# Performance work log

Measured on AMD Instinct MI355X. Metric: run time of the kernel, lower is better.

The kernel has to match this reference:

```python
import jax, jax.numpy as jnp
import numpy as np
import math

D_KEY = 64
SCALE = math.sqrt(D_KEY)
INF = 1e10  # finite stand-in for the original INF constant
CAUSAL = True
DIAG = False


def setup_inputs() -> dict:
    key = jax.random.key(0)
    kq, kk, kv = jax.random.split(key, 3)
    B, L, D = 16, 2048, D_KEY
    return {
        "query": jax.random.normal(kq, (B, L, D), dtype=jnp.float32),
        "key": jax.random.normal(kk, (B, L, D), dtype=jnp.float32),
        "value": jax.random.normal(kv, (B, L, D), dtype=jnp.float32),
    }


def reference(query, key, value):
    # scores: [B, Lq, Lk]
    scores = jnp.einsum("bqd,bkd->bqk", query, key)
    L = key.shape[1]
    if CAUSAL:
        # subtract INF above the diagonal (strict upper triangle), as in torch triu(1)
        tri = jnp.triu(jnp.full((L, L), INF, dtype=scores.dtype), k=1)
        scores = scores - tri[None, :, :]
    if DIAG:
        # original scatters -INF onto the diagonal along dim 1
        diag_mask = jnp.eye(L, dtype=bool)
        scores = jnp.where(diag_mask[None, :, :], -INF, scores)
    # softmax over keys after scaling; dropout with p=0.0 is identity
    attn = jax.nn.softmax(scores / SCALE, axis=-1)
    return jnp.einsum("bqk,bkd->bqd", attn, value)
```

## Files before the change

kernel.cpp:

```cpp
#include <hip/hip_runtime.h>

typedef __bf16 bf16_t;
typedef __bf16 bf16x4 __attribute__((ext_vector_type(4)));
typedef __bf16 bf16x8 __attribute__((ext_vector_type(8)));
typedef float  f32x4  __attribute__((ext_vector_type(4)));

#define B_SZ  16
#define L_SEQ 2048
#define D_H   64
#define QB    64
#define KB    128

#define QSCALE 0.18033688011112043f

__global__ __launch_bounds__(256, 2)
void attn_fwd_kernel(const float* __restrict__ Qg, const float* __restrict__ Kg,
                     const float* __restrict__ Vg, float* __restrict__ Og)
{
    const int lin  = blockIdx.x;
    const int xcd  = lin & 7;
    const int slot = lin >> 3;
    const int half = slot >> 5;
    const int qi   = slot & 31;
    const int b    = xcd * 2 + half;
    const int qt   = half ? qi : (31 - qi);

    const int tid  = threadIdx.x;
    const int lane = tid & 63;
    const int lg   = lane >> 4;
    const int lc   = lane & 15;
    const int lc7  = lc & 7;

    __shared__ __align__(16) bf16_t K_lds[2][KB * D_H];
    __shared__ __align__(16) bf16_t Vt_lds[2][D_H * KB];

    const size_t bbase = (size_t)b * L_SEQ * D_H;

    const int qrow = qt * QB + (tid >> 6) * 16 + lc;
    bf16x8 qa[2];
#pragma unroll
    for (int h = 0; h < 2; ++h) {
        const float* qp = Qg + bbase + (size_t)qrow * D_H + h * 32 + lg * 8;
        const f32x4 f0 = *reinterpret_cast<const f32x4*>(qp);
        const f32x4 f1 = *reinterpret_cast<const f32x4*>(qp + 4);
        bf16x8 a;
#pragma unroll
        for (int j = 0; j < 4; ++j) { a[j] = (bf16_t)(f0[j] * QSCALE); a[4 + j] = (bf16_t)(f1[j] * QSCALE); }
        qa[h] = a;
    }

    f32x4 o[4];
#pragma unroll
    for (int dt = 0; dt < 4; ++dt) o[dt] = (f32x4){0.f, 0.f, 0.f, 0.f};
    float m = -1e30f, l = 0.f;

    const int nkt = (qt + 2) >> 1;

    const int vkb  = tid & 31;
    const int vdg  = tid >> 5;
    const int vpos = ((vkb >> 3) << 5) + ((vkb & 3) << 3) + (((vkb >> 2) & 1) << 2);

    f32x4 kreg[8], vreg[8];

    auto issueK = [&](int kt) {
        const int kbase = kt * KB;
#pragma unroll
        for (int i = 0; i < 4; ++i) {
            const int u = i * 256 + tid;
            const int r = u >> 3, ch = u & 7;
            const float* p = Kg + bbase + (size_t)(kbase + r) * D_H + ch * 8;
            kreg[2 * i]     = *reinterpret_cast<const f32x4*>(p);
            kreg[2 * i + 1] = *reinterpret_cast<const f32x4*>(p + 4);
        }
    };
    auto issueV = [&](int kt) {
        const int kbase = kt * KB;
#pragma unroll
        for (int d2 = 0; d2 < 2; ++d2)
#pragma unroll
            for (int i = 0; i < 4; ++i)
                vreg[d2 * 4 + i] = *reinterpret_cast<const f32x4*>(
                    Vg + bbase + (size_t)(kbase + vkb * 4 + i) * D_H + (vdg + d2 * 8) * 4);
    };
    auto writeK = [&](int buf) {
#pragma unroll
        for (int i = 0; i < 4; ++i) {
            const int u = i * 256 + tid;
            const int r = u >> 3, ch = u & 7;
            bf16x8 kk;
#pragma unroll
            for (int j = 0; j < 4; ++j) { kk[j] = (bf16_t)kreg[2 * i][j]; kk[4 + j] = (bf16_t)kreg[2 * i + 1][j]; }
            *reinterpret_cast<bf16x8*>(&K_lds[buf][r * 64 + ((ch ^ (r & 7)) << 3)]) = kk;
        }
    };
    auto writeV = [&](int buf) {
#pragma unroll
        for (int d2 = 0; d2 < 2; ++d2) {
            const int db = vdg + d2 * 8;
#pragma unroll
            for (int j = 0; j < 4; ++j) {
                const int d = db * 4 + j;
                bf16x4 cj = { (bf16_t)vreg[d2 * 4 + 0][j], (bf16_t)vreg[d2 * 4 + 1][j],
                              (bf16_t)vreg[d2 * 4 + 2][j], (bf16_t)vreg[d2 * 4 + 3][j] };
                const int hw = d * 128 + (((vpos >> 3) ^ (d & 7)) << 3) + (vpos & 7);
                *reinterpret_cast<bf16x4*>(&Vt_lds[buf][hw]) = cj;
            }
        }
    };

    issueK(0); issueV(0); writeK(0); writeV(0);
    __syncthreads();
    int cur = 0;
    for (int kt = 0; kt < nkt; ++kt) {
        const bool last = (kt == nkt - 1);
        const int kbase = kt * KB;
        if (!last) issueK(kt + 1);

        f32x4 sc[8];
        __builtin_amdgcn_s_setprio(1);
#pragma unroll
        for (int n = 0; n < 8; ++n) {
            f32x4 acc = (f32x4){0.f, 0.f, 0.f, 0.f};
#pragma unroll
            for (int h = 0; h < 2; ++h) {
                const int hw = (n * 16 + lc) * 64 + ((((h << 2) | lg) ^ lc7) << 3);
                const bf16x8 kb = *reinterpret_cast<const bf16x8*>(&K_lds[cur][hw]);
                acc = __builtin_amdgcn_mfma_f32_16x16x32_bf16(kb, qa[h], acc, 0, 0, 0);
            }
            sc[n] = acc;
        }
        __builtin_amdgcn_s_setprio(0);
        if (!last) issueV(kt + 1);
        if (last) {
#pragma unroll
            for (int n = 0; n < 8; ++n)
#pragma unroll
                for (int r = 0; r < 4; ++r)
                    if (kbase + n * 16 + lg * 4 + r > qrow) sc[n][r] = -1e30f;
        }

        float mxp = fmaxf(fmaxf(sc[0][0], sc[0][1]), fmaxf(sc[0][2], sc[0][3]));
#pragma unroll
        for (int n = 1; n < 8; ++n)
            mxp = fmaxf(mxp, fmaxf(fmaxf(sc[n][0], sc[n][1]), fmaxf(sc[n][2], sc[n][3])));
        if (!__all(mxp <= m + 8.0f)) {
            float mx = mxp;
            mx = fmaxf(mx, __shfl_xor(mx, 16));
            mx = fmaxf(mx, __shfl_xor(mx, 32));
            const float mn = fmaxf(m, mx);
            const float alpha = exp2f(m - mn);
            m = mn;
            l *= alpha;
#pragma unroll
            for (int dt = 0; dt < 4; ++dt)
#pragma unroll
                for (int r = 0; r < 4; ++r) o[dt][r] *= alpha;
        }
        bf16x8 w[4];
        float rs = 0.f;
#pragma unroll
        for (int n = 0; n < 8; ++n) {
            const float p0 = exp2f(sc[n][0] - m), p1 = exp2f(sc[n][1] - m);
            const float p2 = exp2f(sc[n][2] - m), p3 = exp2f(sc[n][3] - m);
            rs += (p0 + p1) + (p2 + p3);
            const int wi = n >> 1, off = (n & 1) * 4;
            w[wi][off + 0] = (bf16_t)p0; w[wi][off + 1] = (bf16_t)p1;
            w[wi][off + 2] = (bf16_t)p2; w[wi][off + 3] = (bf16_t)p3;
        }
        l += rs;

        if (!last) writeK(cur ^ 1);

        __builtin_amdgcn_s_setprio(1);
#pragma unroll
        for (int ks = 0; ks < 4; ++ks) {
#pragma unroll
            for (int dt = 0; dt < 4; ++dt) {
                const int hw = (dt * 16 + lc) * 128 + ((((ks << 2) | lg) ^ lc7) << 3);
                const bf16x8 vb = *reinterpret_cast<const bf16x8*>(&Vt_lds[cur][hw]);
                o[dt] = __builtin_amdgcn_mfma_f32_16x16x32_bf16(vb, w[ks], o[dt], 0, 0, 0);
            }
        }
        __builtin_amdgcn_s_setprio(0);

        if (!last) writeV(cur ^ 1);
        __syncthreads();
        cur ^= 1;
    }

    float lr = l;
    lr += __shfl_xor(lr, 16);
    lr += __shfl_xor(lr, 32);
    const float inv = 1.0f / lr;
#pragma unroll
    for (int dt = 0; dt < 4; ++dt) {
        f32x4 val = { o[dt][0] * inv, o[dt][1] * inv, o[dt][2] * inv, o[dt][3] * inv };
        *reinterpret_cast<f32x4*>(Og + bbase + (size_t)qrow * D_H + dt * 16 + lg * 4) = val;
    }
}

extern "C" void kernel_launch(void* const* d_in, const int* in_sizes, int n_in,
                              void* d_out, int out_size, void* d_ws, size_t ws_size,
                              hipStream_t stream)
{
    const float* Q = (const float*)d_in[0];
    const float* K = (const float*)d_in[1];
    const float* V = (const float*)d_in[2];
    float* O = (float*)d_out;
    attn_fwd_kernel<<<dim3(512), dim3(256), 0, stream>>>(Q, K, V, O);
}
```

Measured before the change: 40.14 us.

## Pre-convert K/V to swizzled bf16 images and stream them via global_load_lds

Adds a preprocessing kernel that converts K and V to bf16 once per call. It writes them into workspace already in the swizzled LDS tile layout, with V transposed. The attention kernel then copies each tile straight from global memory to LDS with global_load_lds, dropping the register staging and per-tile conversion that were repeated by every Q block. This costs an extra kernel launch and a workspace round trip, and the V transpose in the preprocess uses strided scalar reads. A fallback path keeps the original kernel for when the workspace is too small.

Result: slower. 43.28 us (+7.8%).

```diff
diff --git a/kernel.cpp b/kernel.cpp
--- a/kernel.cpp
+++ b/kernel.cpp
@@ -10,12 +10,56 @@
 #define D_H   64
 #define QB    64
 #define KB    128
+#define NTILE 16
+#define TILE_HW (KB * D_H)
 
 #define QSCALE 0.18033688011112043f
 
+#define GLD_LDS16(g, l) __builtin_amdgcn_global_load_lds(                       \
+    (const __attribute__((address_space(1))) void*)(g),                         \
+    (__attribute__((address_space(3))) void*)(l), 16, 0, 0)
+
+__global__ __launch_bounds__(256)
+void preproc_kernel(const float* __restrict__ Kg, const float* __restrict__ Vg,
+                    bf16_t* __restrict__ Kimg, bf16_t* __restrict__ Vimg)
+{
+    const int kt = blockIdx.x, b = blockIdx.y;
+    const int t  = threadIdx.x;
+    const size_t src = (size_t)b * L_SEQ * D_H + (size_t)kt * KB * D_H;
+    bf16_t* ko = Kimg + (size_t)(b * NTILE + kt) * TILE_HW;
+    bf16_t* vo = Vimg + (size_t)(b * NTILE + kt) * TILE_HW;
+
+#pragma unroll
+    for (int i = 0; i < 4; ++i) {
+        const int u = i * 256 + t, r = u >> 3, ch = u & 7;
+        const float* p = Kg + src + r * 64 + ch * 8;
+        const f32x4 a = *reinterpret_cast<const f32x4*>(p);
+        const f32x4 c = *reinterpret_cast<const f32x4*>(p + 4);
+        bf16x8 kk;
+#pragma unroll
+        for (int j = 0; j < 4; ++j) { kk[j] = (bf16_t)a[j]; kk[4 + j] = (bf16_t)c[j]; }
+        *reinterpret_cast<bf16x8*>(&ko[r * 64 + ((ch ^ (r & 7)) << 3)]) = kk;
+    }
+
+    const int d = t & 63, pcg = t >> 6;
+#pragma unroll
+    for (int i = 0; i < 4; ++i) {
+        const int pc = pcg * 4 + i;
+        bf16x8 vv;
+#pragma unroll
+        for (int pw = 0; pw < 8; ++pw) {
+            const int pos = pc * 8 + pw;
+            const int vkb = ((pos >> 3) & 3) | (((pos >> 2) & 1) << 2) | (((pos >> 5) & 3) << 3);
+            const int k   = (vkb << 2) | (pos & 3);
+            vv[pw] = (bf16_t)Vg[src + (size_t)k * 64 + d];
+        }
+        *reinterpret_cast<bf16x8*>(&vo[d * 128 + ((pc ^ (d & 7)) << 3)]) = vv;
+    }
+}
+
 __global__ __launch_bounds__(256, 2)
-void attn_fwd_kernel(const float* __restrict__ Qg, const float* __restrict__ Kg,
-                     const float* __restrict__ Vg, float* __restrict__ Og)
+void attn_fwd_kernel(const float* __restrict__ Qg, float* __restrict__ Og,
+                     const bf16_t* __restrict__ Kimg, const bf16_t* __restrict__ Vimg)
 {
     const int lin  = blockIdx.x;
     const int xcd  = lin & 7;
@@ -26,17 +70,20 @@
     const int qt   = half ? qi : (31 - qi);
 
     const int tid  = threadIdx.x;
+    const int wave = tid >> 6;
     const int lane = tid & 63;
     const int lg   = lane >> 4;
     const int lc   = lane & 15;
     const int lc7  = lc & 7;
 
-    __shared__ __align__(16) bf16_t K_lds[2][KB * D_H];
-    __shared__ __align__(16) bf16_t Vt_lds[2][D_H * KB];
+    __shared__ __align__(16) bf16_t K_lds[2][TILE_HW];
+    __shared__ __align__(16) bf16_t Vt_lds[2][TILE_HW];
 
     const size_t bbase = (size_t)b * L_SEQ * D_H;
-
-    const int qrow = qt * QB + (tid >> 6) * 16 + lc;
+    const bf16_t* kbase_img = Kimg + (size_t)b * NTILE * TILE_HW;
+    const bf16_t* vbase_img = Vimg + (size_t)b * NTILE * TILE_HW;
+
+    const int qrow = qt * QB + wave * 16 + lc;
     bf16x8 qa[2];
 #pragma unroll
     for (int h = 0; h < 2; ++h) {
@@ -56,65 +103,24 @@
 
     const int nkt = (qt + 2) >> 1;
 
-    const int vkb  = tid & 31;
-    const int vdg  = tid >> 5;
-    const int vpos = ((vkb >> 3) << 5) + ((vkb & 3) << 3) + (((vkb >> 2) & 1) << 2);
-
-    f32x4 kreg[8], vreg[8];
-
-    auto issueK = [&](int kt) {
-        const int kbase = kt * KB;
+    auto stage = [&](int kt, int buf) {
+        const bf16_t* ks = kbase_img + (size_t)kt * TILE_HW;
+        const bf16_t* vs = vbase_img + (size_t)kt * TILE_HW;
 #pragma unroll
         for (int i = 0; i < 4; ++i) {
-            const int u = i * 256 + tid;
-            const int r = u >> 3, ch = u & 7;
-            const float* p = Kg + bbase + (size_t)(kbase + r) * D_H + ch * 8;
-            kreg[2 * i]     = *reinterpret_cast<const f32x4*>(p);
-            kreg[2 * i + 1] = *reinterpret_cast<const f32x4*>(p + 4);
-        }
-    };
-    auto issueV = [&](int kt) {
-        const int kbase = kt * KB;
-#pragma unroll
-        for (int d2 = 0; d2 < 2; ++d2)
-#pragma unroll
-            for (int i = 0; i < 4; ++i)
-                vreg[d2 * 4 + i] = *reinterpret_cast<const f32x4*>(
-                    Vg + bbase + (size_t)(kbase + vkb * 4 + i) * D_H + (vdg + d2 * 8) * 4);
-    };
-    auto writeK = [&](int buf) {
-#pragma unroll
-        for (int i = 0; i < 4; ++i) {
-            const int u = i * 256 + tid;
-            const int r = u >> 3, ch = u & 7;
-            bf16x8 kk;
-#pragma unroll
-            for (int j = 0; j < 4; ++j) { kk[j] = (bf16_t)kreg[2 * i][j]; kk[4 + j] = (bf16_t)kreg[2 * i + 1][j]; }
-            *reinterpret_cast<bf16x8*>(&K_lds[buf][r * 64 + ((ch ^ (r & 7)) << 3)]) = kk;
-        }
-    };
-    auto writeV = [&](int buf) {
-#pragma unroll
-        for (int d2 = 0; d2 < 2; ++d2) {
-            const int db = vdg + d2 * 8;
-#pragma unroll
-            for (int j = 0; j < 4; ++j) {
-                const int d = db * 4 + j;
-                bf16x4 cj = { (bf16_t)vreg[d2 * 4 + 0][j], (bf16_t)vreg[d2 * 4 + 1][j],
-                              (bf16_t)vreg[d2 * 4 + 2][j], (bf16_t)vreg[d2 * 4 + 3][j] };
-                const int hw = d * 128 + (((vpos >> 3) ^ (d & 7)) << 3) + (vpos & 7);
-                *reinterpret_cast<bf16x4*>(&Vt_lds[buf][hw]) = cj;
-            }
-        }
-    };
-
-    issueK(0); issueV(0); writeK(0); writeV(0);
+            const int c = wave * 4 + i;
+            GLD_LDS16(ks + c * 512 + lane * 8, &K_lds[buf][c * 512]);
+            GLD_LDS16(vs + c * 512 + lane * 8, &Vt_lds[buf][c * 512]);
+        }
+    };
+
+    stage(0, 0);
     __syncthreads();
     int cur = 0;
     for (int kt = 0; kt < nkt; ++kt) {
         const bool last = (kt == nkt - 1);
-        const int kbase = kt * KB;
-        if (!last) issueK(kt + 1);
+        const int kb0 = kt * KB;
+        if (!last) stage(kt + 1, cur ^ 1);
 
         f32x4 sc[8];
         __builtin_amdgcn_s_setprio(1);
@@ -124,19 +130,18 @@
 #pragma unroll
             for (int h = 0; h < 2; ++h) {
                 const int hw = (n * 16 + lc) * 64 + ((((h << 2) | lg) ^ lc7) << 3);
-                const bf16x8 kb = *reinterpret_cast<const bf16x8*>(&K_lds[cur][hw]);
-                acc = __builtin_amdgcn_mfma_f32_16x16x32_bf16(kb, qa[h], acc, 0, 0, 0);
+                const bf16x8 kkb = *reinterpret_cast<const bf16x8*>(&K_lds[cur][hw]);
+                acc = __builtin_amdgcn_mfma_f32_16x16x32_bf16(kkb, qa[h], acc, 0, 0, 0);
             }
             sc[n] = acc;
         }
         __builtin_amdgcn_s_setprio(0);
-        if (!last) issueV(kt + 1);
         if (last) {
 #pragma unroll
             for (int n = 0; n < 8; ++n)
 #pragma unroll
                 for (int r = 0; r < 4; ++r)
-                    if (kbase + n * 16 + lg * 4 + r > qrow) sc[n][r] = -1e30f;
+                    if (kb0 + n * 16 + lg * 4 + r > qrow) sc[n][r] = -1e30f;
         }
 
         float mxp = fmaxf(fmaxf(sc[0][0], sc[0][1]), fmaxf(sc[0][2], sc[0][3]));
@@ -169,8 +174,6 @@
         }
         l += rs;
 
-        if (!last) writeK(cur ^ 1);
-
         __builtin_amdgcn_s_setprio(1);
 #pragma unroll
         for (int ks = 0; ks < 4; ++ks) {
@@ -183,11 +186,180 @@
         }
         __builtin_amdgcn_s_setprio(0);
 
+        __syncthreads();
+        cur ^= 1;
+    }
+
+    float lr = l;
+    lr += __shfl_xor(lr, 16);
+    lr += __shfl_xor(lr, 32);
+    const float inv = 1.0f / lr;
+#pragma unroll
+    for (int dt = 0; dt < 4; ++dt) {
+        f32x4 val = { o[dt][0] * inv, o[dt][1] * inv, o[dt][2] * inv, o[dt][3] * inv };
+        *reinterpret_cast<f32x4*>(Og + bbase + (size_t)qrow * D_H + dt * 16 + lg * 4) = val;
+    }
+}
+
+__global__ __launch_bounds__(256, 2)
+void attn_fwd_fb(const float* __restrict__ Qg, const float* __restrict__ Kg,
+                 const float* __restrict__ Vg, float* __restrict__ Og)
+{
+    const int lin  = blockIdx.x;
+    const int xcd  = lin & 7;
+    const int slot = lin >> 3;
+    const int half = slot >> 5;
+    const int qi   = slot & 31;
+    const int b    = xcd * 2 + half;
+    const int qt   = half ? qi : (31 - qi);
+
+    const int tid  = threadIdx.x;
+    const int lane = tid & 63;
+    const int lg   = lane >> 4;
+    const int lc   = lane & 15;
+    const int lc7  = lc & 7;
+
+    __shared__ __align__(16) bf16_t K_lds[2][KB * D_H];
+    __shared__ __align__(16) bf16_t Vt_lds[2][D_H * KB];
+
+    const size_t bbase = (size_t)b * L_SEQ * D_H;
+    const int qrow = qt * QB + (tid >> 6) * 16 + lc;
+    bf16x8 qa[2];
+#pragma unroll
+    for (int h = 0; h < 2; ++h) {
+        const float* qp = Qg + bbase + (size_t)qrow * D_H + h * 32 + lg * 8;
+        const f32x4 f0 = *reinterpret_cast<const f32x4*>(qp);
+        const f32x4 f1 = *reinterpret_cast<const f32x4*>(qp + 4);
+        bf16x8 a;
+#pragma unroll
+        for (int j = 0; j < 4; ++j) { a[j] = (bf16_t)(f0[j] * QSCALE); a[4 + j] = (bf16_t)(f1[j] * QSCALE); }
+        qa[h] = a;
+    }
+    f32x4 o[4];
+#pragma unroll
+    for (int dt = 0; dt < 4; ++dt) o[dt] = (f32x4){0.f, 0.f, 0.f, 0.f};
+    float m = -1e30f, l = 0.f;
+    const int nkt = (qt + 2) >> 1;
+    const int vkb  = tid & 31;
+    const int vdg  = tid >> 5;
+    const int vpos = ((vkb >> 3) << 5) + ((vkb & 3) << 3) + (((vkb >> 2) & 1) << 2);
+    f32x4 kreg[8], vreg[8];
+
+    auto issueK = [&](int kt) {
+        const int kbase = kt * KB;
+#pragma unroll
+        for (int i = 0; i < 4; ++i) {
+            const int u = i * 256 + tid;
+            const int r = u >> 3, ch = u & 7;
+            const float* p = Kg + bbase + (size_t)(kbase + r) * D_H + ch * 8;
+            kreg[2 * i]     = *reinterpret_cast<const f32x4*>(p);
+            kreg[2 * i + 1] = *reinterpret_cast<const f32x4*>(p + 4);
+        }
+    };
+    auto issueV = [&](int kt) {
+        const int kbase = kt * KB;
+#pragma unroll
+        for (int d2 = 0; d2 < 2; ++d2)
+#pragma unroll
+            for (int i = 0; i < 4; ++i)
+                vreg[d2 * 4 + i] = *reinterpret_cast<const f32x4*>(
+                    Vg + bbase + (size_t)(kbase + vkb * 4 + i) * D_H + (vdg + d2 * 8) * 4);
+    };
+    auto writeK = [&](int buf) {
+#pragma unroll
+        for (int i = 0; i < 4; ++i) {
+            const int u = i * 256 + tid;
+            const int r = u >> 3, ch = u & 7;
+            bf16x8 kk;
+#pragma unroll
+            for (int j = 0; j < 4; ++j) { kk[j] = (bf16_t)kreg[2 * i][j]; kk[4 + j] = (bf16_t)kreg[2 * i + 1][j]; }
+            *reinterpret_cast<bf16x8*>(&K_lds[buf][r * 64 + ((ch ^ (r & 7)) << 3)]) = kk;
+        }
+    };
+    auto writeV = [&](int buf) {
+#pragma unroll
+        for (int d2 = 0; d2 < 2; ++d2) {
+            const int db = vdg + d2 * 8;
+#pragma unroll
+            for (int j = 0; j < 4; ++j) {
+                const int d = db * 4 + j;
+                bf16x4 cj = { (bf16_t)vreg[d2 * 4 + 0][j], (bf16_t)vreg[d2 * 4 + 1][j],
+                              (bf16_t)vreg[d2 * 4 + 2][j], (bf16_t)vreg[d2 * 4 + 3][j] };
+                const int hw = d * 128 + (((vpos >> 3) ^ (d & 7)) << 3) + (vpos & 7);
+                *reinterpret_cast<bf16x4*>(&Vt_lds[buf][hw]) = cj;
+            }
+        }
+    };
+
+    issueK(0); issueV(0); writeK(0); writeV(0);
+    __syncthreads();
+    int cur = 0;
+    for (int kt = 0; kt < nkt; ++kt) {
+        const bool last = (kt == nkt - 1);
+        const int kbase = kt * KB;
+        if (!last) issueK(kt + 1);
+        f32x4 sc[8];
+#pragma unroll
+        for (int n = 0; n < 8; ++n) {
+            f32x4 acc = (f32x4){0.f, 0.f, 0.f, 0.f};
+#pragma unroll
+            for (int h = 0; h < 2; ++h) {
+                const int hw = (n * 16 + lc) * 64 + ((((h << 2) | lg) ^ lc7) << 3);
+                const bf16x8 kkb = *reinterpret_cast<const bf16x8*>(&K_lds[cur][hw]);
+                acc = __builtin_amdgcn_mfma_f32_16x16x32_bf16(kkb, qa[h], acc, 0, 0, 0);
+            }
+            sc[n] = acc;
+        }
+        if (!last) issueV(kt + 1);
+        if (last) {
+#pragma unroll
+            for (int n = 0; n < 8; ++n)
+#pragma unroll
+                for (int r = 0; r < 4; ++r)
+                    if (kbase + n * 16 + lg * 4 + r > qrow) sc[n][r] = -1e30f;
+        }
+        float mxp = fmaxf(fmaxf(sc[0][0], sc[0][1]), fmaxf(sc[0][2], sc[0][3]));
+#pragma unroll
+        for (int n = 1; n < 8; ++n)
+            mxp = fmaxf(mxp, fmaxf(fmaxf(sc[n][0], sc[n][1]), fmaxf(sc[n][2], sc[n][3])));
+        if (!__all(mxp <= m + 8.0f)) {
+            float mx = mxp;
+            mx = fmaxf(mx, __shfl_xor(mx, 16));
+            mx = fmaxf(mx, __shfl_xor(mx, 32));
+            const float mn = fmaxf(m, mx);
+            const float alpha = exp2f(m - mn);
+            m = mn; l *= alpha;
+#pragma unroll
+            for (int dt = 0; dt < 4; ++dt)
+#pragma unroll
+                for (int r = 0; r < 4; ++r) o[dt][r] *= alpha;
+        }
+        bf16x8 w[4];
+        float rs = 0.f;
+#pragma unroll
+        for (int n = 0; n < 8; ++n) {
+            const float p0 = exp2f(sc[n][0] - m), p1 = exp2f(sc[n][1] - m);
+            const float p2 = exp2f(sc[n][2] - m), p3 = exp2f(sc[n][3] - m);
+            rs += (p0 + p1) + (p2 + p3);
+            const int wi = n >> 1, off = (n & 1) * 4;
+            w[wi][off + 0] = (bf16_t)p0; w[wi][off + 1] = (bf16_t)p1;
+            w[wi][off + 2] = (bf16_t)p2; w[wi][off + 3] = (bf16_t)p3;
+        }
+        l += rs;
+        if (!last) writeK(cur ^ 1);
+#pragma unroll
+        for (int ks = 0; ks < 4; ++ks) {
+#pragma unroll
+            for (int dt = 0; dt < 4; ++dt) {
+                const int hw = (dt * 16 + lc) * 128 + ((((ks << 2) | lg) ^ lc7) << 3);
+                const bf16x8 vb = *reinterpret_cast<const bf16x8*>(&Vt_lds[cur][hw]);
+                o[dt] = __builtin_amdgcn_mfma_f32_16x16x32_bf16(vb, w[ks], o[dt], 0, 0, 0);
+            }
+        }
         if (!last) writeV(cur ^ 1);
         __syncthreads();
         cur ^= 1;
     }
-
     float lr = l;
     lr += __shfl_xor(lr, 16);
     lr += __shfl_xor(lr, 32);
@@ -207,5 +379,15 @@
     const float* K = (const float*)d_in[1];
     const float* V = (const float*)d_in[2];
     float* O = (float*)d_out;
-    attn_fwd_kernel<<<dim3(512), dim3(256), 0, stream>>>(Q, K, V, O);
+
+    const size_t img_elems = (size_t)B_SZ * NTILE * TILE_HW;
+    const size_t need = 2 * img_elems * sizeof(bf16_t);
+    if (ws_size >= need) {
+        bf16_t* Kimg = (bf16_t*)d_ws;
+        bf16_t* Vimg = Kimg + img_elems;
+        preproc_kernel<<<dim3(NTILE, B_SZ), dim3(256), 0, stream>>>(K, V, Kimg, Vimg);
+        attn_fwd_kernel<<<dim3(512), dim3(256), 0, stream>>>(Q, O, Kimg, Vimg);
+    } else {
+        attn_fwd_fb<<<dim3(512), dim3(256), 0, stream>>>(Q, K, V, O);
+    }
 }
```
